# Performance work log

Measured on AMD Instinct MI355X. Metric: run time of the kernel, lower is better.

## Reference

```python
import jax, jax.numpy as jnp
import numpy as np

ALPHAS = (0.1, 0.3, 0.6)
WEIGHTS = (0.5, 0.3, 0.2)
HUBER_MARGIN = 1.0
B, S = 2048, 8192


def setup_inputs() -> dict:
    key = jax.random.key(0)
    k1, k2 = jax.random.split(key)
    pred = jax.random.normal(k1, (B, S), dtype=jnp.float32)
    target = jax.random.normal(k2, (B, S), dtype=jnp.float32)
    return {"pred": pred, "target": target}


def _ema(x, alpha):
    # x: [B, S]; ema[0] = x[0]; ema[i] = alpha*x[i] + (1-alpha)*ema[i-1]
    x0 = x[:, 0]
    def step(carry, xi):
        nc = alpha * xi + (1.0 - alpha) * carry
        return nc, nc
    _, ys = jax.lax.scan(step, x0, x[:, 1:].T)  # ys: [S-1, B]
    return jnp.concatenate([x0[:, None], ys.T], axis=1)  # [B, S]


def _huber_loss(pred_delta, target_delta):
    dir_agreement = pred_delta * target_delta
    step_err = jnp.abs(pred_delta - target_delta)
    quad = jnp.square(jnp.maximum(HUBER_MARGIN - dir_agreement, 0.0)) / (2.0 * HUBER_MARGIN)
    return jnp.where(dir_agreement < 0, step_err, quad).mean(axis=1)  # [B]


def reference(pred, target):
    loss = jnp.zeros((pred.shape[0],), dtype=pred.dtype)
    for alpha, weight in zip(ALPHAS, WEIGHTS):
        pe = _ema(pred, alpha)
        te = _ema(target, alpha)
        pd = pe[:, 1:] - pe[:, :-1]
        td = te[:, 1:] - te[:, :-1]
        loss = loss + weight * _huber_loss(pd, td)
    return loss.mean()  # reduction='mean'
```

## Files before the change

### kernel.cpp

```cpp
#include <hip/hip_runtime.h>

#define B_ROWS 2048
#define S_LEN 8192
#define PER_LANE 32
#define TILE_ELEMS (64 * PER_LANE)
#define NTILES (S_LEN / TILE_ELEMS)
#define WPB 4
#define NBLOCKS (B_ROWS / WPB)

constexpr double cpowi(double b, int e) { double r = 1.0; for (int i = 0; i < e; ++i) r *= b; return r; }
constexpr float tof(double x) { return (x < 1.2e-38 && x > -1.2e-38) ? 0.0f : (float)x; }

#define A0f 0.1f
#define A1f 0.3f
#define A2f 0.6f

constexpr float D0_1 = tof(cpowi(0.9, 32)),  D0_2 = tof(cpowi(0.9, 64)),  D0_4 = tof(cpowi(0.9, 128));
constexpr float D0_8 = tof(cpowi(0.9, 256)), D0_16 = tof(cpowi(0.9, 512)), D0_32 = tof(cpowi(0.9, 1024));
constexpr float D1_1 = tof(cpowi(0.7, 32)),  D1_2 = tof(cpowi(0.7, 64)),  D1_4 = tof(cpowi(0.7, 128));
constexpr float D1_8 = tof(cpowi(0.7, 256)), D1_16 = tof(cpowi(0.7, 512)), D1_32 = tof(cpowi(0.7, 1024));
constexpr float D2_1 = tof(cpowi(0.4, 32)),  D2_2 = tof(cpowi(0.4, 64)),  D2_4 = tof(cpowi(0.4, 128));
constexpr float D2_8 = tof(cpowi(0.4, 256)), D2_16 = tof(cpowi(0.4, 512)), D2_32 = tof(cpowi(0.4, 1024));

__device__ __forceinline__ float ema_scan(float v, int lane,
                                          float d1, float d2, float d4,
                                          float d8, float d16, float d32) {
    float u;
    u = __shfl_up(v, 1);  v += (lane >= 1  ? d1  : 0.0f) * u;
    u = __shfl_up(v, 2);  v += (lane >= 2  ? d2  : 0.0f) * u;
    u = __shfl_up(v, 4);  v += (lane >= 4  ? d4  : 0.0f) * u;
    u = __shfl_up(v, 8);  v += (lane >= 8  ? d8  : 0.0f) * u;
    u = __shfl_up(v, 16); v += (lane >= 16 ? d16 : 0.0f) * u;
    u = __shfl_up(v, 32); v += (lane >= 32 ? d32 : 0.0f) * u;
    return v;
}

__device__ __forceinline__ float huber(float pd, float td) {
    float dir = pd * td;
    float se  = fabsf(pd - td);
    float mm  = fmaxf(1.0f - dir, 0.0f);
    float q   = 0.5f * mm * mm;
    return dir < 0.0f ? se : q;
}

__global__ void __launch_bounds__(256) msl_main(const float* __restrict__ pred,
                                                const float* __restrict__ targ,
                                                float* __restrict__ partial) {
    const int lane = threadIdx.x & 63;
    const int wave = threadIdx.x >> 6;
    const int row  = blockIdx.x * WPB + wave;
    const float* __restrict__ prow = pred + (size_t)row * S_LEN;
    const float* __restrict__ trow = targ + (size_t)row * S_LEN;

    float sp0 = 0.f, sp1 = 0.f, sp2 = 0.f, st0 = 0.f, st1 = 0.f, st2 = 0.f;
    float acc0 = 0.f, acc1 = 0.f, acc2 = 0.f;

    for (int tile = 0; tile < NTILES; ++tile) {
        const int base = tile * TILE_ELEMS + lane * PER_LANE;
        float xp[PER_LANE], xt[PER_LANE];
        const float4* p4 = reinterpret_cast<const float4*>(prow + base);
        const float4* t4 = reinterpret_cast<const float4*>(trow + base);
#pragma unroll
        for (int j = 0; j < PER_LANE / 4; ++j) {
            float4 a = p4[j];
            float4 b = t4[j];
            xp[4 * j + 0] = a.x; xp[4 * j + 1] = a.y; xp[4 * j + 2] = a.z; xp[4 * j + 3] = a.w;
            xt[4 * j + 0] = b.x; xt[4 * j + 1] = b.y; xt[4 * j + 2] = b.z; xt[4 * j + 3] = b.w;
        }

        const bool first = (tile == 0);
        const bool lz    = (lane == 0);

        float Lp0 = lz ? (first ? xp[0] : sp0) : 0.0f;
        float Lp1 = lz ? (first ? xp[0] : sp1) : 0.0f;
        float Lp2 = lz ? (first ? xp[0] : sp2) : 0.0f;
        float Lt0 = lz ? (first ? xt[0] : st0) : 0.0f;
        float Lt1 = lz ? (first ? xt[0] : st1) : 0.0f;
        float Lt2 = lz ? (first ? xt[0] : st2) : 0.0f;
#pragma unroll
        for (int j = 0; j < PER_LANE; ++j) {
            Lp0 += A0f * (xp[j] - Lp0);
            Lp1 += A1f * (xp[j] - Lp1);
            Lp2 += A2f * (xp[j] - Lp2);
            Lt0 += A0f * (xt[j] - Lt0);
            Lt1 += A1f * (xt[j] - Lt1);
            Lt2 += A2f * (xt[j] - Lt2);
        }

        float vp0 = ema_scan(Lp0, lane, D0_1, D0_2, D0_4, D0_8, D0_16, D0_32);
        float vp1 = ema_scan(Lp1, lane, D1_1, D1_2, D1_4, D1_8, D1_16, D1_32);
        float vp2 = ema_scan(Lp2, lane, D2_1, D2_2, D2_4, D2_8, D2_16, D2_32);
        float vt0 = ema_scan(Lt0, lane, D0_1, D0_2, D0_4, D0_8, D0_16, D0_32);
        float vt1 = ema_scan(Lt1, lane, D1_1, D1_2, D1_4, D1_8, D1_16, D1_32);
        float vt2 = ema_scan(Lt2, lane, D2_1, D2_2, D2_4, D2_8, D2_16, D2_32);

        float cp0 = __shfl_up(vp0, 1), cp1 = __shfl_up(vp1, 1), cp2 = __shfl_up(vp2, 1);
        float ct0 = __shfl_up(vt0, 1), ct1 = __shfl_up(vt1, 1), ct2 = __shfl_up(vt2, 1);

        float yp0 = lz ? (first ? xp[0] : sp0) : cp0;
        float yp1 = lz ? (first ? xp[0] : sp1) : cp1;
        float yp2 = lz ? (first ? xp[0] : sp2) : cp2;
        float yt0 = lz ? (first ? xt[0] : st0) : ct0;
        float yt1 = lz ? (first ? xt[0] : st1) : ct1;
        float yt2 = lz ? (first ? xt[0] : st2) : ct2;

        sp0 = __shfl(vp0, 63); sp1 = __shfl(vp1, 63); sp2 = __shfl(vp2, 63);
        st0 = __shfl(vt0, 63); st1 = __shfl(vt1, 63); st2 = __shfl(vt2, 63);

        const float skip = (first && lz) ? 0.0f : 1.0f;
#pragma unroll
        for (int j = 0; j < PER_LANE; ++j) {
            float pd0 = A0f * (xp[j] - yp0); yp0 += pd0;
            float td0 = A0f * (xt[j] - yt0); yt0 += td0;
            float pd1 = A1f * (xp[j] - yp1); yp1 += pd1;
            float td1 = A1f * (xt[j] - yt1); yt1 += td1;
            float pd2 = A2f * (xp[j] - yp2); yp2 += pd2;
            float td2 = A2f * (xt[j] - yt2); yt2 += td2;

            float h0 = huber(pd0, td0);
            float h1 = huber(pd1, td1);
            float h2 = huber(pd2, td2);
            if (j == 0) { h0 *= skip; h1 *= skip; h2 *= skip; }
            acc0 += h0; acc1 += h1; acc2 += h2;
        }
    }

    float wacc = 0.5f * acc0 + 0.3f * acc1 + 0.2f * acc2;
#pragma unroll
    for (int o = 32; o > 0; o >>= 1) wacc += __shfl_down(wacc, o);

    __shared__ float sred[WPB];
    if (lane == 0) sred[wave] = wacc;
    __syncthreads();
    if (threadIdx.x == 0)
        partial[blockIdx.x] = sred[0] + sred[1] + sred[2] + sred[3];
}

__global__ void __launch_bounds__(256) msl_reduce(const float* __restrict__ partial,
                                                  float* __restrict__ out) {
    const int tid = threadIdx.x;
    float v = partial[tid] + partial[tid + 256];
#pragma unroll
    for (int o = 32; o > 0; o >>= 1) v += __shfl_down(v, o);
    __shared__ float s[4];
    if ((tid & 63) == 0) s[tid >> 6] = v;
    __syncthreads();
    if (tid == 0)
        out[0] = (s[0] + s[1] + s[2] + s[3]) *
                 (float)(1.0 / ((double)(S_LEN - 1) * (double)B_ROWS));
}

extern "C" void kernel_launch(void* const* d_in, const int* in_sizes, int n_in,
                              void* d_out, int out_size, void* d_ws, size_t ws_size,
                              hipStream_t stream) {
    const float* pred = (const float*)d_in[0];
    const float* targ = (const float*)d_in[1];
    float* out = (float*)d_out;
    float* partial = (float*)d_ws;

    msl_main<<<NBLOCKS, 256, 0, stream>>>(pred, targ, partial);
    msl_reduce<<<1, 256, 0, stream>>>(partial, out);
}
```

Measured before the change: 154.1 us.

## Split each row across eight waves with a cross-wave EMA carry fixup

Each row was previously processed by one wave walking 4 sequential tiles, with the EMA carry passed between tiles. Now a 512-thread block owns one row and each of its 8 waves takes a 1024-element chunk with 16 elements per lane. Wave-local scans are combined through shared memory, and each lane applies the previous wave's carry with decay weights computed by exp2f. This removes the serial tile loop and raises parallelism and memory-level parallelism, at the cost of a block barrier, a transcendental per lane, and a truncated carry (only the immediately preceding wave's carry is applied; this relies on the decay over 1024 steps underflowing to zero).

New measurement: 144.9 us. 1.06x faster.

```diff
diff --git a/kernel.cpp b/kernel.cpp
--- a/kernel.cpp
+++ b/kernel.cpp
@@ -1,12 +1,11 @@
 #include <hip/hip_runtime.h>
 
 #define B_ROWS 2048
-#define S_LEN 8192
-#define PER_LANE 32
-#define TILE_ELEMS (64 * PER_LANE)
-#define NTILES (S_LEN / TILE_ELEMS)
-#define WPB 4
-#define NBLOCKS (B_ROWS / WPB)
+#define S_LEN  8192
+#define PER_LANE 16
+#define WPB 8
+#define CHUNK (64 * PER_LANE)
+#define NBLOCKS B_ROWS
 
 constexpr double cpowi(double b, int e) { double r = 1.0; for (int i = 0; i < e; ++i) r *= b; return r; }
 constexpr float tof(double x) { return (x < 1.2e-38 && x > -1.2e-38) ? 0.0f : (float)x; }
@@ -15,12 +14,16 @@
 #define A1f 0.3f
 #define A2f 0.6f
 
-constexpr float D0_1 = tof(cpowi(0.9, 32)),  D0_2 = tof(cpowi(0.9, 64)),  D0_4 = tof(cpowi(0.9, 128));
-constexpr float D0_8 = tof(cpowi(0.9, 256)), D0_16 = tof(cpowi(0.9, 512)), D0_32 = tof(cpowi(0.9, 1024));
-constexpr float D1_1 = tof(cpowi(0.7, 32)),  D1_2 = tof(cpowi(0.7, 64)),  D1_4 = tof(cpowi(0.7, 128));
-constexpr float D1_8 = tof(cpowi(0.7, 256)), D1_16 = tof(cpowi(0.7, 512)), D1_32 = tof(cpowi(0.7, 1024));
-constexpr float D2_1 = tof(cpowi(0.4, 32)),  D2_2 = tof(cpowi(0.4, 64)),  D2_4 = tof(cpowi(0.4, 128));
-constexpr float D2_8 = tof(cpowi(0.4, 256)), D2_16 = tof(cpowi(0.4, 512)), D2_32 = tof(cpowi(0.4, 1024));
+constexpr float D0_1 = tof(cpowi(0.9, 16)),  D0_2 = tof(cpowi(0.9, 32)),  D0_4 = tof(cpowi(0.9, 64));
+constexpr float D0_8 = tof(cpowi(0.9, 128)), D0_16 = tof(cpowi(0.9, 256)), D0_32 = tof(cpowi(0.9, 512));
+constexpr float D1_1 = tof(cpowi(0.7, 16)),  D1_2 = tof(cpowi(0.7, 32)),  D1_4 = tof(cpowi(0.7, 64));
+constexpr float D1_8 = tof(cpowi(0.7, 128)), D1_16 = tof(cpowi(0.7, 256)), D1_32 = tof(cpowi(0.7, 512));
+constexpr float D2_1 = tof(cpowi(0.4, 16)),  D2_2 = tof(cpowi(0.4, 32)),  D2_4 = tof(cpowi(0.4, 64));
+constexpr float D2_8 = tof(cpowi(0.4, 128)), D2_16 = tof(cpowi(0.4, 256)), D2_32 = tof(cpowi(0.4, 512));
+
+#define L2_0 (-0.15200309344504997f)
+#define L2_1 (-0.51457317282975830f)
+#define L2_2 (-1.32192809488736230f)
 
 __device__ __forceinline__ float ema_scan(float v, int lane,
                                           float d1, float d2, float d4,
@@ -43,86 +46,97 @@
     return dir < 0.0f ? se : q;
 }
 
-__global__ void __launch_bounds__(256) msl_main(const float* __restrict__ pred,
+__global__ void __launch_bounds__(512) msl_main(const float* __restrict__ pred,
                                                 const float* __restrict__ targ,
                                                 float* __restrict__ partial) {
     const int lane = threadIdx.x & 63;
     const int wave = threadIdx.x >> 6;
-    const int row  = blockIdx.x * WPB + wave;
-    const float* __restrict__ prow = pred + (size_t)row * S_LEN;
-    const float* __restrict__ trow = targ + (size_t)row * S_LEN;
+    const float* __restrict__ prow = pred + (size_t)blockIdx.x * S_LEN;
+    const float* __restrict__ trow = targ + (size_t)blockIdx.x * S_LEN;
+    const int base = wave * CHUNK + lane * PER_LANE;
 
-    float sp0 = 0.f, sp1 = 0.f, sp2 = 0.f, st0 = 0.f, st1 = 0.f, st2 = 0.f;
+    float xp[PER_LANE], xt[PER_LANE];
+    const float4* p4 = reinterpret_cast<const float4*>(prow + base);
+    const float4* t4 = reinterpret_cast<const float4*>(trow + base);
+#pragma unroll
+    for (int j = 0; j < PER_LANE / 4; ++j) {
+        float4 a = p4[j];
+        float4 b = t4[j];
+        xp[4 * j + 0] = a.x; xp[4 * j + 1] = a.y; xp[4 * j + 2] = a.z; xp[4 * j + 3] = a.w;
+        xt[4 * j + 0] = b.x; xt[4 * j + 1] = b.y; xt[4 * j + 2] = b.z; xt[4 * j + 3] = b.w;
+    }
+
+    const bool w0   = (wave == 0);
+    const bool lz   = (lane == 0);
+    const bool head = w0 && lz;
+
+    float Lp0 = head ? xp[0] : 0.0f;
+    float Lp1 = head ? xp[0] : 0.0f;
+    float Lp2 = head ? xp[0] : 0.0f;
+    float Lt0 = head ? xt[0] : 0.0f;
+    float Lt1 = head ? xt[0] : 0.0f;
+    float Lt2 = head ? xt[0] : 0.0f;
+#pragma unroll
+    for (int j = 0; j < PER_LANE; ++j) {
+        Lp0 += A0f * (xp[j] - Lp0);
+        Lp1 += A1f * (xp[j] - Lp1);
+        Lp2 += A2f * (xp[j] - Lp2);
+        Lt0 += A0f * (xt[j] - Lt0);
+        Lt1 += A1f * (xt[j] - Lt1);
+        Lt2 += A2f * (xt[j] - Lt2);
+    }
+
+    float vp0 = ema_scan(Lp0, lane, D0_1, D0_2, D0_4, D0_8, D0_16, D0_32);
+    float vp1 = ema_scan(Lp1, lane, D1_1, D1_2, D1_4, D1_8, D1_16, D1_32);
+    float vp2 = ema_scan(Lp2, lane, D2_1, D2_2, D2_4, D2_8, D2_16, D2_32);
+    float vt0 = ema_scan(Lt0, lane, D0_1, D0_2, D0_4, D0_8, D0_16, D0_32);
+    float vt1 = ema_scan(Lt1, lane, D1_1, D1_2, D1_4, D1_8, D1_16, D1_32);
+    float vt2 = ema_scan(Lt2, lane, D2_1, D2_2, D2_4, D2_8, D2_16, D2_32);
+
+    __shared__ float sex[WPB][6];
+    if (lane == 63) {
+        sex[wave][0] = vp0; sex[wave][1] = vp1; sex[wave][2] = vp2;
+        sex[wave][3] = vt0; sex[wave][4] = vt1; sex[wave][5] = vt2;
+    }
+    __syncthreads();
+
+    float Cp0 = 0.f, Cp1 = 0.f, Cp2 = 0.f, Ct0 = 0.f, Ct1 = 0.f, Ct2 = 0.f;
+    if (wave > 0) {
+        Cp0 = sex[wave - 1][0]; Cp1 = sex[wave - 1][1]; Cp2 = sex[wave - 1][2];
+        Ct0 = sex[wave - 1][3]; Ct1 = sex[wave - 1][4]; Ct2 = sex[wave - 1][5];
+    }
+
+    const float e  = (float)(PER_LANE * lane);
+    const float W0 = exp2f(e * L2_0);
+    const float W1 = exp2f(e * L2_1);
+    const float W2 = exp2f(e * L2_2);
+
+    float up0 = __shfl_up(vp0, 1), up1 = __shfl_up(vp1, 1), up2 = __shfl_up(vp2, 1);
+    float ut0 = __shfl_up(vt0, 1), ut1 = __shfl_up(vt1, 1), ut2 = __shfl_up(vt2, 1);
+
+    float yp0 = lz ? (w0 ? xp[0] : Cp0) : fmaf(W0, Cp0, up0);
+    float yp1 = lz ? (w0 ? xp[0] : Cp1) : fmaf(W1, Cp1, up1);
+    float yp2 = lz ? (w0 ? xp[0] : Cp2) : fmaf(W2, Cp2, up2);
+    float yt0 = lz ? (w0 ? xt[0] : Ct0) : fmaf(W0, Ct0, ut0);
+    float yt1 = lz ? (w0 ? xt[0] : Ct1) : fmaf(W1, Ct1, ut1);
+    float yt2 = lz ? (w0 ? xt[0] : Ct2) : fmaf(W2, Ct2, ut2);
+
     float acc0 = 0.f, acc1 = 0.f, acc2 = 0.f;
+    const float skip = head ? 0.0f : 1.0f;
+#pragma unroll
+    for (int j = 0; j < PER_LANE; ++j) {
+        float pd0 = A0f * (xp[j] - yp0); yp0 += pd0;
+        float td0 = A0f * (xt[j] - yt0); yt0 += td0;
+        float pd1 = A1f * (xp[j] - yp1); yp1 += pd1;
+        float td1 = A1f * (xt[j] - yt1); yt1 += td1;
+        float pd2 = A2f * (xp[j] - yp2); yp2 += pd2;
+        float td2 = A2f * (xt[j] - yt2); yt2 += td2;
 
-    for (int tile = 0; tile < NTILES; ++tile) {
-        const int base = tile * TILE_ELEMS + lane * PER_LANE;
-        float xp[PER_LANE], xt[PER_LANE];
-        const float4* p4 = reinterpret_cast<const float4*>(prow + base);
-        const float4* t4 = reinterpret_cast<const float4*>(trow + base);
-#pragma unroll
-        for (int j = 0; j < PER_LANE / 4; ++j) {
-            float4 a = p4[j];
-            float4 b = t4[j];
-            xp[4 * j + 0] = a.x; xp[4 * j + 1] = a.y; xp[4 * j + 2] = a.z; xp[4 * j + 3] = a.w;
-            xt[4 * j + 0] = b.x; xt[4 * j + 1] = b.y; xt[4 * j + 2] = b.z; xt[4 * j + 3] = b.w;
-        }
-
-        const bool first = (tile == 0);
-        const bool lz    = (lane == 0);
-
-        float Lp0 = lz ? (first ? xp[0] : sp0) : 0.0f;
-        float Lp1 = lz ? (first ? xp[0] : sp1) : 0.0f;
-        float Lp2 = lz ? (first ? xp[0] : sp2) : 0.0f;
-        float Lt0 = lz ? (first ? xt[0] : st0) : 0.0f;
-        float Lt1 = lz ? (first ? xt[0] : st1) : 0.0f;
-        float Lt2 = lz ? (first ? xt[0] : st2) : 0.0f;
-#pragma unroll
-        for (int j = 0; j < PER_LANE; ++j) {
-            Lp0 += A0f * (xp[j] - Lp0);
-            Lp1 += A1f * (xp[j] - Lp1);
-            Lp2 += A2f * (xp[j] - Lp2);
-            Lt0 += A0f * (xt[j] - Lt0);
-            Lt1 += A1f * (xt[j] - Lt1);
-            Lt2 += A2f * (xt[j] - Lt2);
-        }
-
-        float vp0 = ema_scan(Lp0, lane, D0_1, D0_2, D0_4, D0_8, D0_16, D0_32);
-        float vp1 = ema_scan(Lp1, lane, D1_1, D1_2, D1_4, D1_8, D1_16, D1_32);
-        float vp2 = ema_scan(Lp2, lane, D2_1, D2_2, D2_4, D2_8, D2_16, D2_32);
-        float vt0 = ema_scan(Lt0, lane, D0_1, D0_2, D0_4, D0_8, D0_16, D0_32);
-        float vt1 = ema_scan(Lt1, lane, D1_1, D1_2, D1_4, D1_8, D1_16, D1_32);
-        float vt2 = ema_scan(Lt2, lane, D2_1, D2_2, D2_4, D2_8, D2_16, D2_32);
-
-        float cp0 = __shfl_up(vp0, 1), cp1 = __shfl_up(vp1, 1), cp2 = __shfl_up(vp2, 1);
-        float ct0 = __shfl_up(vt0, 1), ct1 = __shfl_up(vt1, 1), ct2 = __shfl_up(vt2, 1);
-
-        float yp0 = lz ? (first ? xp[0] : sp0) : cp0;
-        float yp1 = lz ? (first ? xp[0] : sp1) : cp1;
-        float yp2 = lz ? (first ? xp[0] : sp2) : cp2;
-        float yt0 = lz ? (first ? xt[0] : st0) : ct0;
-        float yt1 = lz ? (first ? xt[0] : st1) : ct1;
-        float yt2 = lz ? (first ? xt[0] : st2) : ct2;
-
-        sp0 = __shfl(vp0, 63); sp1 = __shfl(vp1, 63); sp2 = __shfl(vp2, 63);
-        st0 = __shfl(vt0, 63); st1 = __shfl(vt1, 63); st2 = __shfl(vt2, 63);
-
-        const float skip = (first && lz) ? 0.0f : 1.0f;
-#pragma unroll
-        for (int j = 0; j < PER_LANE; ++j) {
-            float pd0 = A0f * (xp[j] - yp0); yp0 += pd0;
-            float td0 = A0f * (xt[j] - yt0); yt0 += td0;
-            float pd1 = A1f * (xp[j] - yp1); yp1 += pd1;
-            float td1 = A1f * (xt[j] - yt1); yt1 += td1;
-            float pd2 = A2f * (xp[j] - yp2); yp2 += pd2;
-            float td2 = A2f * (xt[j] - yt2); yt2 += td2;
-
-            float h0 = huber(pd0, td0);
-            float h1 = huber(pd1, td1);
-            float h2 = huber(pd2, td2);
-            if (j == 0) { h0 *= skip; h1 *= skip; h2 *= skip; }
-            acc0 += h0; acc1 += h1; acc2 += h2;
-        }
+        float h0 = huber(pd0, td0);
+        float h1 = huber(pd1, td1);
+        float h2 = huber(pd2, td2);
+        if (j == 0) { h0 *= skip; h1 *= skip; h2 *= skip; }
+        acc0 += h0; acc1 += h1; acc2 += h2;
     }
 
     float wacc = 0.5f * acc0 + 0.3f * acc1 + 0.2f * acc2;
@@ -130,16 +144,22 @@
     for (int o = 32; o > 0; o >>= 1) wacc += __shfl_down(wacc, o);
 
     __shared__ float sred[WPB];
-    if (lane == 0) sred[wave] = wacc;
+    if (lz) sred[wave] = wacc;
     __syncthreads();
-    if (threadIdx.x == 0)
-        partial[blockIdx.x] = sred[0] + sred[1] + sred[2] + sred[3];
+    if (threadIdx.x == 0) {
+        float s = 0.f;
+#pragma unroll
+        for (int i = 0; i < WPB; ++i) s += sred[i];
+        partial[blockIdx.x] = s;
+    }
 }
 
 __global__ void __launch_bounds__(256) msl_reduce(const float* __restrict__ partial,
                                                   float* __restrict__ out) {
     const int tid = threadIdx.x;
-    float v = partial[tid] + partial[tid + 256];
+    float v = 0.f;
+#pragma unroll
+    for (int k = 0; k < NBLOCKS / 256; ++k) v += partial[tid + 256 * k];
 #pragma unroll
     for (int o = 32; o > 0; o >>= 1) v += __shfl_down(v, o);
     __shared__ float s[4];
@@ -158,6 +178,6 @@
     float* out = (float*)d_out;
     float* partial = (float*)d_ws;
 
-    msl_main<<<NBLOCKS, 256, 0, stream>>>(pred, targ, partial);
+    msl_main<<<NBLOCKS, 512, 0, stream>>>(pred, targ, partial);
     msl_reduce<<<1, 256, 0, stream>>>(partial, out);
 }
```
